# Optimization experiments

Hardware: AMD Instinct MI355X
Metric: run time of the kernel (lower is better)

Reference implementation:

```python
import jax, jax.numpy as jnp
import numpy as np

B, T, NX = 4, 6, 128
F_IN, H, F_OUT = 64, 128, 64
N = T * NX * NX  # 98304 cubed-sphere nodes


def _build_neighbors():
    # 4-neighbor grid adjacency per tile (periodic within tile), [N, 4] int32.
    t = np.arange(T)[:, None, None]
    i = np.arange(NX)[None, :, None]
    j = np.arange(NX)[None, None, :]

    def nid(tt, ii, jj):
        return tt * NX * NX + (ii % NX) * NX + (jj % NX)

    nbr = np.stack(
        [nid(t, i - 1, j), nid(t, i + 1, j), nid(t, i, j - 1), nid(t, i, j + 1)],
        axis=-1,
    ).reshape(-1, 4)
    return jnp.asarray(nbr, dtype=jnp.int32)


def setup_inputs() -> dict:
    key = jax.random.key(0)
    ks = jax.random.split(key, 20)
    inp = {
        "inputs": jax.random.normal(ks[0], (B, T, NX, NX, F_IN), dtype=jnp.float32),
        "nbr": _build_neighbors(),
    }
    # SAGEConv channel chain: 64->128, 128->64, 64->32, 32->32, 64->64, 128->64
    dims = [(F_IN, H), (H, H // 2), (H // 2, H // 4), (H // 4, H // 4), (H // 2, H // 2), (H, F_OUT)]
    k = 1
    for li, (din, dout) in enumerate(dims, start=1):
        s = 1.0 / np.sqrt(din)
        inp[f"W_self_{li}"] = jax.random.normal(ks[k], (din, dout), dtype=jnp.float32) * s
        inp[f"W_neigh_{li}"] = jax.random.normal(ks[k + 1], (din, dout), dtype=jnp.float32) * s
        inp[f"b_{li}"] = jnp.zeros((dout,), dtype=jnp.float32)
        k += 2
    return inp


def _sage(h, nbr, Ws, Wn, b):
    # h: [N, B, F]. Mean over the 4 fixed grid neighbors, then self+neighbor linear.
    m = (h[nbr[:, 0]] + h[nbr[:, 1]] + h[nbr[:, 2]] + h[nbr[:, 3]]) * 0.25
    return h @ Ws + m @ Wn + b


def reference(inputs, nbr,
              W_self_1, W_neigh_1, b_1, W_self_2, W_neigh_2, b_2,
              W_self_3, W_neigh_3, b_3, W_self_4, W_neigh_4, b_4,
              W_self_5, W_neigh_5, b_5, W_self_6, W_neigh_6, b_6):
    b, t, nx, ny, f = inputs.shape
    x = inputs.reshape(b, t * nx * ny, f).transpose(1, 0, 2)  # [N, B, F]
    act = jax.nn.relu
    # num_blocks = 1
    h1 = act(_sage(x, nbr, W_self_1, W_neigh_1, b_1))
    h2 = act(_sage(h1, nbr, W_self_2, W_neigh_2, b_2))
    h3 = act(_sage(h2, nbr, W_self_3, W_neigh_3, b_3))
    h4 = act(_sage(h3, nbr, W_self_4, W_neigh_4, b_4))
    h5 = jnp.concatenate([act(_sage(h4, nbr, W_self_4, W_neigh_4, b_4)), h3], axis=-1)
    h6 = jnp.concatenate([act(_sage(h5, nbr, W_self_5, W_neigh_5, b_5)), h2], axis=-1)
    out = _sage(h6, nbr, W_self_6, W_neigh_6, b_6)  # [N, B, F_OUT]
    return out.transpose(1, 0, 2).reshape(b, t, nx, ny, -1)
```

## Files before the change

### kernel.cpp

```cpp
#include <hip/hip_runtime.h>

#define NNODES 98304
#define NB 4
#define NTILES ((NNODES * NB) / 64)
#define GRID_BLOCKS 1024

typedef __attribute__((ext_vector_type(8))) short short8;
typedef __attribute__((ext_vector_type(8))) unsigned short ushort8;
typedef __attribute__((ext_vector_type(4))) float f32x4;

__device__ __forceinline__ float bf2f(unsigned short u) {
  union { unsigned int u; float f; } c; c.u = ((unsigned int)u) << 16; return c.f;
}
__device__ __forceinline__ unsigned short f2bf(float f) {
  union { float f; unsigned int u; } c; c.f = f;
  unsigned int r = 0x7FFFu + ((c.u >> 16) & 1u);
  return (unsigned short)((c.u + r) >> 16);
}
__device__ __forceinline__ unsigned int cvtpk(float lo, float hi) {
  unsigned int r;
  asm("v_cvt_pk_bf16_f32 %0, %1, %2" : "=v"(r) : "v"(lo), "v"(hi));
  return r;
}

template<int FIN, int FOUT, int SRCK, int DSTK, bool RELU>
__global__ __launch_bounds__(256, 4)
void sage_mfma(const void* __restrict__ srcp, int sstride, int soff,
               void* __restrict__ dstp, int dstride, int doff,
               const float* __restrict__ Ws, const float* __restrict__ Wn,
               const float* __restrict__ bias, const int* __restrict__ nbr)
{
  constexpr int K = 2 * FIN;
  constexpr int KSTEPS = K / 32;
  constexpr int LD = K + 8;
  constexpr int WAVES_N = (FOUT >= 64) ? 4 : 2;
  constexpr int WAVES_M = 4 / WAVES_N;
  constexpr int CF = FOUT / (16 * WAVES_N);
  constexpr int RF = 64 / (16 * WAVES_M);

  __shared__ unsigned short As[64][LD];

  const int tid = threadIdx.x;
  const int wave = tid >> 6;
  const int lane = tid & 63;
  const int wn = wave % WAVES_N;
  const int wm = wave / WAVES_N;
  const int colbase = wn * (FOUT / WAVES_N);
  const int rowbase = wm * (64 / WAVES_M);
  const int fn = lane & 15;
  const int fg = lane >> 4;

  short8 Bfrag[KSTEPS][CF];
  float bv[CF];
  #pragma unroll
  for (int ks = 0; ks < KSTEPS; ++ks) {
    const float* wb = (ks * 32 < FIN) ? (Ws + (size_t)(ks * 32) * FOUT)
                                      : (Wn + (size_t)(ks * 32 - FIN) * FOUT);
    #pragma unroll
    for (int cf = 0; cf < CF; ++cf) {
      const int col = colbase + cf * 16 + fn;
      short8 f;
      #pragma unroll
      for (int j = 0; j < 8; ++j)
        f[j] = (short)f2bf(wb[(size_t)(fg * 8 + j) * FOUT + col]);
      Bfrag[ks][cf] = f;
    }
  }
  #pragma unroll
  for (int cf = 0; cf < CF; ++cf) bv[cf] = bias[colbase + cf * 16 + fn];

  for (int tile = blockIdx.x; tile < NTILES; tile += GRID_BLOCKS) {
    const int node0 = tile * 16;

    constexpr int CHUNKS = FIN / 8;
    constexpr int ITERS = (64 * CHUNKS) / 256;
    #pragma unroll
    for (int it = 0; it < ITERS; ++it) {
      const int g = tid + it * 256;
      const int r = g / CHUNKS;
      const int c = (g - r * CHUNKS) * 8;
      const int n = node0 + (r >> 2);
      const int b = r & 3;
      const int4 nb4 = reinterpret_cast<const int4*>(nbr)[n];
      uint4 xv, mv;
      if (SRCK == 0) {
        const float* s = (const float*)srcp;
        const float* ps = s + ((size_t)b * NNODES + n) * FIN + c;
        const float* p0 = s + ((size_t)b * NNODES + nb4.x) * FIN + c;
        const float* p1 = s + ((size_t)b * NNODES + nb4.y) * FIN + c;
        const float* p2 = s + ((size_t)b * NNODES + nb4.z) * FIN + c;
        const float* p3 = s + ((size_t)b * NNODES + nb4.w) * FIN + c;
        float4 sa = *(const float4*)ps,        sb = *(const float4*)(ps + 4);
        float4 a0 = *(const float4*)p0,        b0 = *(const float4*)(p0 + 4);
        float4 a1 = *(const float4*)p1,        b1 = *(const float4*)(p1 + 4);
        float4 a2 = *(const float4*)p2,        b2 = *(const float4*)(p2 + 4);
        float4 a3 = *(const float4*)p3,        b3 = *(const float4*)(p3 + 4);
        xv = make_uint4(cvtpk(sa.x, sa.y), cvtpk(sa.z, sa.w),
                        cvtpk(sb.x, sb.y), cvtpk(sb.z, sb.w));
        float4 m0, m1;
        m0.x = (a0.x + a1.x) + (a2.x + a3.x); m0.y = (a0.y + a1.y) + (a2.y + a3.y);
        m0.z = (a0.z + a1.z) + (a2.z + a3.z); m0.w = (a0.w + a1.w) + (a2.w + a3.w);
        m1.x = (b0.x + b1.x) + (b2.x + b3.x); m1.y = (b0.y + b1.y) + (b2.y + b3.y);
        m1.z = (b0.z + b1.z) + (b2.z + b3.z); m1.w = (b0.w + b1.w) + (b2.w + b3.w);
        mv = make_uint4(cvtpk(m0.x * 0.25f, m0.y * 0.25f), cvtpk(m0.z * 0.25f, m0.w * 0.25f),
                        cvtpk(m1.x * 0.25f, m1.y * 0.25f), cvtpk(m1.z * 0.25f, m1.w * 0.25f));
      } else {
        const unsigned short* s = (const unsigned short*)srcp;
        auto ld = [&](int nn) {
          return *reinterpret_cast<const ushort8*>(s + ((size_t)nn * NB + b) * sstride + soff + c);
        };
        const ushort8 sv = ld(n);
        xv = make_uint4((unsigned)sv[0] | ((unsigned)sv[1] << 16),
                        (unsigned)sv[2] | ((unsigned)sv[3] << 16),
                        (unsigned)sv[4] | ((unsigned)sv[5] << 16),
                        (unsigned)sv[6] | ((unsigned)sv[7] << 16));
        const ushort8 a0 = ld(nb4.x), a1 = ld(nb4.y), a2 = ld(nb4.z), a3 = ld(nb4.w);
        float sum[8];
        #pragma unroll
        for (int j = 0; j < 8; ++j)
          sum[j] = (bf2f(a0[j]) + bf2f(a1[j])) + (bf2f(a2[j]) + bf2f(a3[j]));
        mv = make_uint4(cvtpk(sum[0] * 0.25f, sum[1] * 0.25f), cvtpk(sum[2] * 0.25f, sum[3] * 0.25f),
                        cvtpk(sum[4] * 0.25f, sum[5] * 0.25f), cvtpk(sum[6] * 0.25f, sum[7] * 0.25f));
      }
      *reinterpret_cast<uint4*>(&As[r][c]) = xv;
      *reinterpret_cast<uint4*>(&As[r][FIN + c]) = mv;
    }
    __syncthreads();

    f32x4 acc[RF][CF];
    #pragma unroll
    for (int rf = 0; rf < RF; ++rf)
      #pragma unroll
      for (int cf = 0; cf < CF; ++cf)
        acc[rf][cf] = (f32x4){bv[cf], bv[cf], bv[cf], bv[cf]};

    #pragma unroll
    for (int ks = 0; ks < KSTEPS; ++ks) {
      short8 a[RF];
      #pragma unroll
      for (int rf = 0; rf < RF; ++rf)
        a[rf] = *reinterpret_cast<const short8*>(&As[rowbase + rf * 16 + fn][ks * 32 + fg * 8]);
      #pragma unroll
      for (int rf = 0; rf < RF; ++rf)
        #pragma unroll
        for (int cf = 0; cf < CF; ++cf)
          acc[rf][cf] = __builtin_amdgcn_mfma_f32_16x16x32_bf16(
              a[rf], Bfrag[ks][cf], acc[rf][cf], 0, 0, 0);
    }
    __syncthreads();

    #pragma unroll
    for (int rf = 0; rf < RF; ++rf) {
      #pragma unroll
      for (int cf = 0; cf < CF; ++cf) {
        const int col = colbase + cf * 16 + fn;
        #pragma unroll
        for (int j = 0; j < 4; ++j) {
          const int row = rowbase + rf * 16 + fg * 4 + j;
          const int n = node0 + (row >> 2);
          const int b = row & 3;
          float v = acc[rf][cf][j];
          if (RELU) v = fmaxf(v, 0.f);
          if (DSTK == 0) {
            ((float*)dstp)[((size_t)b * NNODES + n) * FOUT + col] = v;
          } else {
            ((unsigned short*)dstp)[((size_t)n * NB + b) * dstride + doff + col] = f2bf(v);
          }
        }
      }
    }
  }
}

extern "C" void kernel_launch(void* const* d_in, const int* in_sizes, int n_in,
                              void* d_out, int out_size, void* d_ws, size_t ws_size,
                              hipStream_t stream) {
  const float* x  = (const float*)d_in[0];
  const int* nbr  = (const int*)d_in[1];
  const float* W1s = (const float*)d_in[2],  *W1n = (const float*)d_in[3],  *b1 = (const float*)d_in[4];
  const float* W2s = (const float*)d_in[5],  *W2n = (const float*)d_in[6],  *b2 = (const float*)d_in[7];
  const float* W3s = (const float*)d_in[8],  *W3n = (const float*)d_in[9],  *b3 = (const float*)d_in[10];
  const float* W4s = (const float*)d_in[11], *W4n = (const float*)d_in[12], *b4 = (const float*)d_in[13];
  const float* W5s = (const float*)d_in[14], *W5n = (const float*)d_in[15], *b5 = (const float*)d_in[16];
  const float* W6s = (const float*)d_in[17], *W6n = (const float*)d_in[18], *b6 = (const float*)d_in[19];

  unsigned short* h1 = (unsigned short*)d_out;
  unsigned short* h6 = (unsigned short*)d_ws;
  unsigned short* h5 = (unsigned short*)d_out;
  unsigned short* h4 = (unsigned short*)((char*)d_out + (size_t)NNODES * NB * 64 * 2);

  const dim3 grid(GRID_BLOCKS), block(256);

  sage_mfma<64, 128, 0, 1, true><<<grid, block, 0, stream>>>(x, 0, 0, h1, 128, 0, W1s, W1n, b1, nbr);
  sage_mfma<128, 64, 1, 1, true><<<grid, block, 0, stream>>>(h1, 128, 0, h6, 128, 64, W2s, W2n, b2, nbr);
  sage_mfma<64, 32, 1, 1, true><<<grid, block, 0, stream>>>(h6, 128, 64, h5, 64, 32, W3s, W3n, b3, nbr);
  sage_mfma<32, 32, 1, 1, true><<<grid, block, 0, stream>>>(h5, 64, 32, h4, 32, 0, W4s, W4n, b4, nbr);
  sage_mfma<32, 32, 1, 1, true><<<grid, block, 0, stream>>>(h4, 32, 0, h5, 64, 0, W4s, W4n, b4, nbr);
  sage_mfma<64, 64, 1, 1, true><<<grid, block, 0, stream>>>(h5, 64, 0, h6, 128, 0, W5s, W5n, b5, nbr);
  sage_mfma<128, 64, 1, 0, false><<<grid, block, 0, stream>>>(h6, 128, 0, d_out, 0, 0, W6s, W6n, b6, nbr);
}
```

Measured before the change: 250.5 us.

## Prefetch next tile's gathers during MFMA and vectorize transposed output stores

Software-pipelines the persistent tile loop: global gathers for the next tile are issued before the MFMA phase and finished into LDS after it, so load latency overlaps compute. Swaps the MFMA operand order so each lane holds four consecutive output columns, which allows vectorized float4/packed-bf16 stores and a float4 bias load. The cost is more live registers for the prefetch buffers, which may cut occupancy at launch_bounds(256,4).

```diff
diff --git a/kernel.cpp b/kernel.cpp
--- a/kernel.cpp
+++ b/kernel.cpp
@@ -1,4 +1,5 @@
 #include <hip/hip_runtime.h>
+#include <type_traits>
 
 #define NNODES 98304
 #define NB 4
@@ -37,21 +38,21 @@
   constexpr int WAVES_M = 4 / WAVES_N;
   constexpr int CF = FOUT / (16 * WAVES_N);
   constexpr int RF = 64 / (16 * WAVES_M);
+  constexpr int CHUNKS = FIN / 8;
+  constexpr int ITERS = (64 * CHUNKS) / 256;
+  constexpr int PF = (SRCK == 0) ? 1 : (ITERS < 2 ? ITERS : 2);
+  constexpr int PT = ITERS - PF;
 
   __shared__ unsigned short As[64][LD];
 
   const int tid = threadIdx.x;
-  const int wave = tid >> 6;
-  const int lane = tid & 63;
-  const int wn = wave % WAVES_N;
-  const int wm = wave / WAVES_N;
+  const int wave = tid >> 6, lane = tid & 63;
+  const int wn = wave % WAVES_N, wm = wave / WAVES_N;
   const int colbase = wn * (FOUT / WAVES_N);
   const int rowbase = wm * (64 / WAVES_M);
-  const int fn = lane & 15;
-  const int fg = lane >> 4;
-
-  short8 Bfrag[KSTEPS][CF];
-  float bv[CF];
+  const int fn = lane & 15, fg = lane >> 4;
+
+  short8 Wfrag[KSTEPS][CF];
   #pragma unroll
   for (int ks = 0; ks < KSTEPS; ++ks) {
     const float* wb = (ks * 32 < FIN) ? (Ws + (size_t)(ks * 32) * FOUT)
@@ -63,68 +64,101 @@
       #pragma unroll
       for (int j = 0; j < 8; ++j)
         f[j] = (short)f2bf(wb[(size_t)(fg * 8 + j) * FOUT + col]);
-      Bfrag[ks][cf] = f;
+      Wfrag[ks][cf] = f;
     }
   }
+  float4 bv4[CF];
   #pragma unroll
-  for (int cf = 0; cf < CF; ++cf) bv[cf] = bias[colbase + cf * 16 + fn];
+  for (int cf = 0; cf < CF; ++cf)
+    bv4[cf] = *reinterpret_cast<const float4*>(bias + colbase + cf * 16 + fg * 4);
+
+  struct G0 { float4 s0, s1, a0, a1, b0, b1, c0, c1, d0, d1; };
+  struct G1 { ushort8 s, n0, n1, n2, n3; };
+  using PG = typename std::conditional<SRCK == 0, G0, G1>::type;
+
+  auto issue = [&](int node0, int it, PG& p) {
+    const int g = tid + it * 256;
+    const int r = g / CHUNKS;
+    const int c = (g - r * CHUNKS) * 8;
+    const int n = node0 + (r >> 2);
+    const int b = r & 3;
+    const int4 nb4 = reinterpret_cast<const int4*>(nbr)[n];
+    if constexpr (SRCK == 0) {
+      const float* s = (const float*)srcp;
+      const float* ps = s + ((size_t)b * NNODES + n) * FIN + c;
+      const float* p0 = s + ((size_t)b * NNODES + nb4.x) * FIN + c;
+      const float* p1 = s + ((size_t)b * NNODES + nb4.y) * FIN + c;
+      const float* p2 = s + ((size_t)b * NNODES + nb4.z) * FIN + c;
+      const float* p3 = s + ((size_t)b * NNODES + nb4.w) * FIN + c;
+      p.s0 = *(const float4*)ps; p.s1 = *(const float4*)(ps + 4);
+      p.a0 = *(const float4*)p0; p.a1 = *(const float4*)(p0 + 4);
+      p.b0 = *(const float4*)p1; p.b1 = *(const float4*)(p1 + 4);
+      p.c0 = *(const float4*)p2; p.c1 = *(const float4*)(p2 + 4);
+      p.d0 = *(const float4*)p3; p.d1 = *(const float4*)(p3 + 4);
+    } else {
+      const unsigned short* s = (const unsigned short*)srcp;
+      auto ld = [&](int nn) {
+        return *reinterpret_cast<const ushort8*>(s + ((size_t)nn * NB + b) * sstride + soff + c);
+      };
+      p.s = ld(n); p.n0 = ld(nb4.x); p.n1 = ld(nb4.y); p.n2 = ld(nb4.z); p.n3 = ld(nb4.w);
+    }
+  };
+
+  auto finish = [&](int it, PG& p) {
+    const int g = tid + it * 256;
+    const int r = g / CHUNKS;
+    const int c = (g - r * CHUNKS) * 8;
+    uint4 xv, mv;
+    if constexpr (SRCK == 0) {
+      xv = make_uint4(cvtpk(p.s0.x, p.s0.y), cvtpk(p.s0.z, p.s0.w),
+                      cvtpk(p.s1.x, p.s1.y), cvtpk(p.s1.z, p.s1.w));
+      float4 m0, m1;
+      m0.x = (p.a0.x + p.b0.x) + (p.c0.x + p.d0.x);
+      m0.y = (p.a0.y + p.b0.y) + (p.c0.y + p.d0.y);
+      m0.z = (p.a0.z + p.b0.z) + (p.c0.z + p.d0.z);
+      m0.w = (p.a0.w + p.b0.w) + (p.c0.w + p.d0.w);
+      m1.x = (p.a1.x + p.b1.x) + (p.c1.x + p.d1.x);
+      m1.y = (p.a1.y + p.b1.y) + (p.c1.y + p.d1.y);
+      m1.z = (p.a1.z + p.b1.z) + (p.c1.z + p.d1.z);
+      m1.w = (p.a1.w + p.b1.w) + (p.c1.w + p.d1.w);
+      mv = make_uint4(cvtpk(m0.x * 0.25f, m0.y * 0.25f), cvtpk(m0.z * 0.25f, m0.w * 0.25f),
+                      cvtpk(m1.x * 0.25f, m1.y * 0.25f), cvtpk(m1.z * 0.25f, m1.w * 0.25f));
+    } else {
+      xv = make_uint4((unsigned)(unsigned short)p.s[0] | ((unsigned)(unsigned short)p.s[1] << 16),
+                      (unsigned)(unsigned short)p.s[2] | ((unsigned)(unsigned short)p.s[3] << 16),
+                      (unsigned)(unsigned short)p.s[4] | ((unsigned)(unsigned short)p.s[5] << 16),
+                      (unsigned)(unsigned short)p.s[6] | ((unsigned)(unsigned short)p.s[7] << 16));
+      float sum[8];
+      #pragma unroll
+      for (int j = 0; j < 8; ++j)
+        sum[j] = (bf2f(p.n0[j]) + bf2f(p.n1[j])) + (bf2f(p.n2[j]) + bf2f(p.n3[j]));
+      mv = make_uint4(cvtpk(sum[0] * 0.25f, sum[1] * 0.25f), cvtpk(sum[2] * 0.25f, sum[3] * 0.25f),
+                      cvtpk(sum[4] * 0.25f, sum[5] * 0.25f), cvtpk(sum[6] * 0.25f, sum[7] * 0.25f));
+    }
+    *reinterpret_cast<uint4*>(&As[r][c]) = xv;
+    *reinterpret_cast<uint4*>(&As[r][FIN + c]) = mv;
+  };
+
+  {
+    const int node0 = blockIdx.x * 16;
+    PG p[ITERS];
+    #pragma unroll
+    for (int it = 0; it < ITERS; ++it) issue(node0, it, p[it]);
+    #pragma unroll
+    for (int it = 0; it < ITERS; ++it) finish(it, p[it]);
+  }
 
   for (int tile = blockIdx.x; tile < NTILES; tile += GRID_BLOCKS) {
     const int node0 = tile * 16;
-
-    constexpr int CHUNKS = FIN / 8;
-    constexpr int ITERS = (64 * CHUNKS) / 256;
-    #pragma unroll
-    for (int it = 0; it < ITERS; ++it) {
-      const int g = tid + it * 256;
-      const int r = g / CHUNKS;
-      const int c = (g - r * CHUNKS) * 8;
-      const int n = node0 + (r >> 2);
-      const int b = r & 3;
-      const int4 nb4 = reinterpret_cast<const int4*>(nbr)[n];
-      uint4 xv, mv;
-      if (SRCK == 0) {
-        const float* s = (const float*)srcp;
-        const float* ps = s + ((size_t)b * NNODES + n) * FIN + c;
-        const float* p0 = s + ((size_t)b * NNODES + nb4.x) * FIN + c;
-        const float* p1 = s + ((size_t)b * NNODES + nb4.y) * FIN + c;
-        const float* p2 = s + ((size_t)b * NNODES + nb4.z) * FIN + c;
-        const float* p3 = s + ((size_t)b * NNODES + nb4.w) * FIN + c;
-        float4 sa = *(const float4*)ps,        sb = *(const float4*)(ps + 4);
-        float4 a0 = *(const float4*)p0,        b0 = *(const float4*)(p0 + 4);
-        float4 a1 = *(const float4*)p1,        b1 = *(const float4*)(p1 + 4);
-        float4 a2 = *(const float4*)p2,        b2 = *(const float4*)(p2 + 4);
-        float4 a3 = *(const float4*)p3,        b3 = *(const float4*)(p3 + 4);
-        xv = make_uint4(cvtpk(sa.x, sa.y), cvtpk(sa.z, sa.w),
-                        cvtpk(sb.x, sb.y), cvtpk(sb.z, sb.w));
-        float4 m0, m1;
-        m0.x = (a0.x + a1.x) + (a2.x + a3.x); m0.y = (a0.y + a1.y) + (a2.y + a3.y);
-        m0.z = (a0.z + a1.z) + (a2.z + a3.z); m0.w = (a0.w + a1.w) + (a2.w + a3.w);
-        m1.x = (b0.x + b1.x) + (b2.x + b3.x); m1.y = (b0.y + b1.y) + (b2.y + b3.y);
-        m1.z = (b0.z + b1.z) + (b2.z + b3.z); m1.w = (b0.w + b1.w) + (b2.w + b3.w);
-        mv = make_uint4(cvtpk(m0.x * 0.25f, m0.y * 0.25f), cvtpk(m0.z * 0.25f, m0.w * 0.25f),
-                        cvtpk(m1.x * 0.25f, m1.y * 0.25f), cvtpk(m1.z * 0.25f, m1.w * 0.25f));
-      } else {
-        const unsigned short* s = (const unsigned short*)srcp;
-        auto ld = [&](int nn) {
-          return *reinterpret_cast<const ushort8*>(s + ((size_t)nn * NB + b) * sstride + soff + c);
-        };
-        const ushort8 sv = ld(n);
-        xv = make_uint4((unsigned)sv[0] | ((unsigned)sv[1] << 16),
-                        (unsigned)sv[2] | ((unsigned)sv[3] << 16),
-                        (unsigned)sv[4] | ((unsigned)sv[5] << 16),
-                        (unsigned)sv[6] | ((unsigned)sv[7] << 16));
-        const ushort8 a0 = ld(nb4.x), a1 = ld(nb4.y), a2 = ld(nb4.z), a3 = ld(nb4.w);
-        float sum[8];
-        #pragma unroll
-        for (int j = 0; j < 8; ++j)
-          sum[j] = (bf2f(a0[j]) + bf2f(a1[j])) + (bf2f(a2[j]) + bf2f(a3[j]));
-        mv = make_uint4(cvtpk(sum[0] * 0.25f, sum[1] * 0.25f), cvtpk(sum[2] * 0.25f, sum[3] * 0.25f),
-                        cvtpk(sum[4] * 0.25f, sum[5] * 0.25f), cvtpk(sum[6] * 0.25f, sum[7] * 0.25f));
-      }
-      *reinterpret_cast<uint4*>(&As[r][c]) = xv;
-      *reinterpret_cast<uint4*>(&As[r][FIN + c]) = mv;
-    }
+    const bool hasnext = (tile + GRID_BLOCKS) < NTILES;
+    const int nnode0 = (tile + GRID_BLOCKS) * 16;
+
+    PG ptop[PF];
+    if (hasnext) {
+      #pragma unroll
+      for (int it = 0; it < PF; ++it) issue(nnode0, it, ptop[it]);
+    }
+
     __syncthreads();
 
     f32x4 acc[RF][CF];
@@ -132,7 +166,7 @@
     for (int rf = 0; rf < RF; ++rf)
       #pragma unroll
       for (int cf = 0; cf < CF; ++cf)
-        acc[rf][cf] = (f32x4){bv[cf], bv[cf], bv[cf], bv[cf]};
+        acc[rf][cf] = (f32x4){bv4[cf].x, bv4[cf].y, bv4[cf].z, bv4[cf].w};
 
     #pragma unroll
     for (int ks = 0; ks < KSTEPS; ++ks) {
@@ -145,29 +179,42 @@
         #pragma unroll
         for (int cf = 0; cf < CF; ++cf)
           acc[rf][cf] = __builtin_amdgcn_mfma_f32_16x16x32_bf16(
-              a[rf], Bfrag[ks][cf], acc[rf][cf], 0, 0, 0);
-    }
-    __syncthreads();
+              Wfrag[ks][cf], a[rf], acc[rf][cf], 0, 0, 0);
+    }
 
     #pragma unroll
     for (int rf = 0; rf < RF; ++rf) {
+      const int xrow = rowbase + rf * 16 + fn;
+      const int n = node0 + (xrow >> 2);
+      const int b = xrow & 3;
       #pragma unroll
       for (int cf = 0; cf < CF; ++cf) {
-        const int col = colbase + cf * 16 + fn;
-        #pragma unroll
-        for (int j = 0; j < 4; ++j) {
-          const int row = rowbase + rf * 16 + fg * 4 + j;
-          const int n = node0 + (row >> 2);
-          const int b = row & 3;
-          float v = acc[rf][cf][j];
-          if (RELU) v = fmaxf(v, 0.f);
-          if (DSTK == 0) {
-            ((float*)dstp)[((size_t)b * NNODES + n) * FOUT + col] = v;
-          } else {
-            ((unsigned short*)dstp)[((size_t)n * NB + b) * dstride + doff + col] = f2bf(v);
-          }
+        f32x4 v = acc[rf][cf];
+        if (RELU) {
+          v[0] = fmaxf(v[0], 0.f); v[1] = fmaxf(v[1], 0.f);
+          v[2] = fmaxf(v[2], 0.f); v[3] = fmaxf(v[3], 0.f);
+        }
+        const int col = colbase + cf * 16 + fg * 4;
+        if (DSTK == 0) {
+          float4 o = make_float4(v[0], v[1], v[2], v[3]);
+          *reinterpret_cast<float4*>((float*)dstp + ((size_t)b * NNODES + n) * FOUT + col) = o;
+        } else {
+          uint2 u = make_uint2(cvtpk(v[0], v[1]), cvtpk(v[2], v[3]));
+          *reinterpret_cast<uint2*>((unsigned short*)dstp + ((size_t)n * NB + b) * dstride + doff + col) = u;
         }
       }
+    }
+
+    __syncthreads();
+
+    if (hasnext) {
+      PG ptail[PT > 0 ? PT : 1];
+      #pragma unroll
+      for (int it = 0; it < PT; ++it) issue(nnode0, PF + it, ptail[it]);
+      #pragma unroll
+      for (int it = 0; it < PF; ++it) finish(it, ptop[it]);
+      #pragma unroll
+      for (int it = 0; it < PT; ++it) finish(PF + it, ptail[it]);
     }
   }
 }
```

After: 373.6 us. 1.49x slower.
